# Kernel tuning notes

Measured on AMD Instinct MI355X. Metric: run time of the kernel, lower is better.

The kernel has to match this reference:

```python
import jax, jax.numpy as jnp
import numpy as np

B, IN, HID, EMB, K = 65536, 256, 256, 64, 4096
EPS = 1e-5  # BatchNorm1d default eps


def setup_inputs() -> dict:
    key = jax.random.key(0)
    ks = jax.random.split(key, 12)
    s = 0.05
    return {
        "x": jax.random.normal(ks[0], (B, IN), jnp.float32),
        "W1": jax.random.normal(ks[1], (HID, IN), jnp.float32) * s,
        "b1": jax.random.normal(ks[2], (HID,), jnp.float32) * s,
        "gamma": jnp.ones((HID,), jnp.float32),
        "beta": jnp.zeros((HID,), jnp.float32),
        "mean": jax.random.normal(ks[3], (HID,), jnp.float32) * s,
        "var": jax.random.uniform(ks[4], (HID,), jnp.float32, 0.5, 1.5),
        "W2": jax.random.normal(ks[5], (HID // 2, HID), jnp.float32) * s,
        "b2": jax.random.normal(ks[6], (HID // 2,), jnp.float32) * s,
        "W3": jax.random.normal(ks[7], (EMB, HID // 2), jnp.float32) * s,
        "b3": jax.random.normal(ks[8], (EMB,), jnp.float32) * s,
        "codebook": jax.random.normal(ks[9], (K, EMB), jnp.float32),
    }


def reference(x, W1, b1, gamma, beta, mean, var, W2, b2, W3, b3, codebook):
    # encoder: Linear -> BatchNorm1d (eval stats) -> ReLU -> Linear -> ReLU -> Linear -> Tanh
    h = x @ W1.T + b1                                   # [B, HID]
    h = (h - mean) * jax.lax.rsqrt(var + EPS) * gamma + beta
    h = jax.nn.relu(h)
    h = jax.nn.relu(h @ W2.T + b2)                      # [B, HID//2]
    z = jnp.tanh(h @ W3.T + b3)                         # [B, EMB]
    # squared-distance matrix: ||z||^2 + ||e||^2 - 2 z e^T  -> [B, K]
    d = (jnp.sum(z * z, axis=1, keepdims=True)
         + jnp.sum(codebook * codebook, axis=1)
         - 2.0 * (z @ codebook.T))
    return jnp.argmin(d, axis=1)                        # [B] int token indices
```

## Files before the change

### kernel.cpp

```cpp
#include <hip/hip_runtime.h>

#define IN_DIM  256
#define HID_DIM 256
#define H2_DIM  128
#define EMB_DIM 64
#define K_CODES 4096
#define EPS_BN  1e-5f


typedef _Float16 f16;
typedef _Float16 f16x4 __attribute__((ext_vector_type(4)));
typedef _Float16 f16x8 __attribute__((ext_vector_type(8)));
typedef float    f32x16 __attribute__((ext_vector_type(16)));

__global__ __launch_bounds__(256) void k_norms(const float* __restrict__ cb,
                                               float* __restrict__ norms) {
    int c = blockIdx.x * 256 + threadIdx.x;
    const float4* row = reinterpret_cast<const float4*>(cb + (size_t)c * EMB_DIM);
    float s = 0.f;
#pragma unroll
    for (int i = 0; i < EMB_DIM / 4; ++i) {
        float4 v = row[i];
        s += v.x * v.x + v.y * v.y + v.z * v.z + v.w * v.w;
    }
    norms[c] = 0.5f * s;
}

__global__ __launch_bounds__(256) void k_prep(
    const float* __restrict__ W1, const float* __restrict__ W2,
    const float* __restrict__ W3, const float* __restrict__ cb,
    f16* __restrict__ w1h, f16* __restrict__ w1l,
    f16* __restrict__ w2h, f16* __restrict__ w2l,
    f16* __restrict__ w3h, f16* __restrict__ w3l,
    f16* __restrict__ cbh, f16* __restrict__ cbl) {
    int i = blockIdx.x * 256 + threadIdx.x;
    const float* src; f16 *dh, *dl; int off;
    if (i < 65536)       { src = W1; dh = w1h; dl = w1l; off = i; }
    else if (i < 98304)  { src = W2; dh = w2h; dl = w2l; off = i - 65536; }
    else if (i < 106496) { src = W3; dh = w3h; dl = w3l; off = i - 98304; }
    else                 { src = cb; dh = cbh; dl = cbl; off = i - 106496; }
    float v = src[off];
    f16 h = (f16)v;
    dh[off] = h;
    dl[off] = (f16)(v - (float)h);
}

__global__ __launch_bounds__(256) void k_encoder_mfma(
    const float* __restrict__ x,
    const f16* __restrict__ w1h, const f16* __restrict__ w1l,
    const f16* __restrict__ w2h, const f16* __restrict__ w2l,
    const f16* __restrict__ w3h, const f16* __restrict__ w3l,
    const float* __restrict__ b1,
    const float* __restrict__ gm, const float* __restrict__ bt,
    const float* __restrict__ mu, const float* __restrict__ vr,
    const float* __restrict__ b2, const float* __restrict__ b3,
    f16* __restrict__ Zh, f16* __restrict__ Zl) {
    __shared__ __align__(16) f16 sm[27136];
    const int tid  = threadIdx.x;
    const int lane = tid & 63;
    const int w    = tid >> 6;
    const int ln31 = lane & 31;
    const int q    = lane >> 5;
    const int r0   = blockIdx.x * 32;

    f32x16 acc1a = {};
    f32x16 acc1b = {};
#pragma unroll 1
    for (int kc = 0; kc < 8; ++kc) {
        __syncthreads();
        {
            int row = tid >> 3, c = (tid & 7) * 4;
            float4 v = *reinterpret_cast<const float4*>(
                x + (size_t)(r0 + row) * IN_DIM + kc * 32 + c);
            f16x4 hv, lv;
            hv[0] = (f16)v.x; lv[0] = (f16)(v.x - (float)hv[0]);
            hv[1] = (f16)v.y; lv[1] = (f16)(v.y - (float)hv[1]);
            hv[2] = (f16)v.z; lv[2] = (f16)(v.z - (float)hv[2]);
            hv[3] = (f16)v.w; lv[3] = (f16)(v.w - (float)hv[3]);
            *(f16x4*)(sm + row * 40 + c)        = hv;
            *(f16x4*)(sm + 1280 + row * 40 + c) = lv;
        }
#pragma unroll
        for (int it = 0; it < 4; ++it) {
            int i = it * 256 + tid;
            int j = i >> 2, c8 = (i & 3) * 8;
            *(f16x8*)(sm + 2560 + j * 40 + c8) =
                *(const f16x8*)(w1h + j * IN_DIM + kc * 32 + c8);
            *(f16x8*)(sm + 12800 + j * 40 + c8) =
                *(const f16x8*)(w1l + j * IN_DIM + kc * 32 + c8);
        }
        __syncthreads();
#pragma unroll
        for (int ks = 0; ks < 2; ++ks) {
            f16x8 ah = *(const f16x8*)(sm + ln31 * 40 + ks * 16 + q * 8);
            f16x8 al = *(const f16x8*)(sm + 1280 + ln31 * 40 + ks * 16 + q * 8);
            int j0 = (w * 64 + ln31) * 40 + ks * 16 + q * 8;
            f16x8 bh0 = *(const f16x8*)(sm + 2560 + j0);
            f16x8 bl0 = *(const f16x8*)(sm + 12800 + j0);
            f16x8 bh1 = *(const f16x8*)(sm + 2560 + j0 + 32 * 40);
            f16x8 bl1 = *(const f16x8*)(sm + 12800 + j0 + 32 * 40);
            acc1a = __builtin_amdgcn_mfma_f32_32x32x16_f16(ah, bh0, acc1a, 0, 0, 0);
            acc1b = __builtin_amdgcn_mfma_f32_32x32x16_f16(ah, bh1, acc1b, 0, 0, 0);
            acc1a = __builtin_amdgcn_mfma_f32_32x32x16_f16(al, bh0, acc1a, 0, 0, 0);
            acc1b = __builtin_amdgcn_mfma_f32_32x32x16_f16(al, bh1, acc1b, 0, 0, 0);
            acc1a = __builtin_amdgcn_mfma_f32_32x32x16_f16(ah, bl0, acc1a, 0, 0, 0);
            acc1b = __builtin_amdgcn_mfma_f32_32x32x16_f16(ah, bl1, acc1b, 0, 0, 0);
        }
    }
    __syncthreads();

    {
#pragma unroll
        for (int nt = 0; nt < 2; ++nt) {
            int j = w * 64 + nt * 32 + ln31;
            float sc = gm[j] * rsqrtf(vr[j] + EPS_BN);
            float sh = (b1[j] - mu[j]) * sc + bt[j];
            const f32x16& a = nt ? acc1b : acc1a;
#pragma unroll
            for (int r = 0; r < 16; ++r) {
                int row = (r & 3) + 8 * (r >> 2) + 4 * q;
                float v = a[r] * sc + sh;
                v = v > 0.f ? v : 0.f;
                f16 h = (f16)v;
                sm[row * 264 + j]        = h;
                sm[8448 + row * 264 + j] = (f16)(v - (float)h);
            }
        }
    }

    f32x16 acc2a = {};
    f32x16 acc2b = {};
#pragma unroll 1
    for (int kc = 0; kc < 8; ++kc) {
        __syncthreads();
#pragma unroll
        for (int it = 0; it < 2; ++it) {
            int i = it * 256 + tid;
            int j = i >> 2, c8 = (i & 3) * 8;
            *(f16x8*)(sm + 16896 + j * 40 + c8) =
                *(const f16x8*)(w2h + j * HID_DIM + kc * 32 + c8);
            *(f16x8*)(sm + 22016 + j * 40 + c8) =
                *(const f16x8*)(w2l + j * HID_DIM + kc * 32 + c8);
        }
        __syncthreads();
#pragma unroll
        for (int ks = 0; ks < 2; ++ks) {
            f16x8 ah = *(const f16x8*)(sm + ln31 * 264 + kc * 32 + ks * 16 + q * 8);
            f16x8 al = *(const f16x8*)(sm + 8448 + ln31 * 264 + kc * 32 + ks * 16 + q * 8);
            int j0 = (w * 32 + ln31) * 40 + ks * 16 + q * 8;
            f16x8 bh = *(const f16x8*)(sm + 16896 + j0);
            f16x8 bl = *(const f16x8*)(sm + 22016 + j0);
            f32x16& acc = ks ? acc2b : acc2a;
            acc = __builtin_amdgcn_mfma_f32_32x32x16_f16(ah, bh, acc, 0, 0, 0);
            acc = __builtin_amdgcn_mfma_f32_32x32x16_f16(al, bh, acc, 0, 0, 0);
            acc = __builtin_amdgcn_mfma_f32_32x32x16_f16(ah, bl, acc, 0, 0, 0);
        }
    }
    __syncthreads();

    {
        int j2 = w * 32 + ln31;
        float bias = b2[j2];
#pragma unroll
        for (int r = 0; r < 16; ++r) {
            int row = (r & 3) + 8 * (r >> 2) + 4 * q;
            float v = (acc2a[r] + acc2b[r]) + bias;
            v = v > 0.f ? v : 0.f;
            f16 h = (f16)v;
            sm[row * 136 + j2]        = h;
            sm[4352 + row * 136 + j2] = (f16)(v - (float)h);
        }
#pragma unroll
        for (int it = 0; it < 4; ++it) {
            int i = it * 256 + tid;
            int j = i >> 4, c8 = (i & 15) * 8;
            *(f16x8*)(sm + 8704 + j * 136 + c8) =
                *(const f16x8*)(w3h + j * H2_DIM + c8);
            *(f16x8*)(sm + 17408 + j * 136 + c8) =
                *(const f16x8*)(w3l + j * H2_DIM + c8);
        }
    }
    __syncthreads();

    if (w < 2) {
        f32x16 acc3a = {};
        f32x16 acc3b = {};
#pragma unroll 2
        for (int ks = 0; ks < 8; ++ks) {
            f16x8 ah = *(const f16x8*)(sm + ln31 * 136 + ks * 16 + q * 8);
            f16x8 al = *(const f16x8*)(sm + 4352 + ln31 * 136 + ks * 16 + q * 8);
            int j0 = 8704 + (w * 32 + ln31) * 136 + ks * 16 + q * 8;
            f16x8 bh = *(const f16x8*)(sm + j0);
            f16x8 bl = *(const f16x8*)(sm + j0 + 8704);
            f32x16& acc = (ks & 1) ? acc3b : acc3a;
            acc = __builtin_amdgcn_mfma_f32_32x32x16_f16(ah, bh, acc, 0, 0, 0);
            acc = __builtin_amdgcn_mfma_f32_32x32x16_f16(al, bh, acc, 0, 0, 0);
            acc = __builtin_amdgcn_mfma_f32_32x32x16_f16(ah, bl, acc, 0, 0, 0);
        }
        int j3 = w * 32 + ln31;
        float bias = b3[j3];
#pragma unroll
        for (int r = 0; r < 16; ++r) {
            int row = (r & 3) + 8 * (r >> 2) + 4 * q;
            float zv = tanhf((acc3a[r] + acc3b[r]) + bias);
            f16 h = (f16)zv;
            size_t idx = (size_t)(r0 + row) * EMB_DIM + j3;
            Zh[idx] = h;
            Zl[idx] = (f16)(zv - (float)h);
        }
    }
}

__global__ __launch_bounds__(256) void k_argmin_mfma(
    const f16* __restrict__ Zh, const f16* __restrict__ Zl,
    const f16* __restrict__ cbh, const f16* __restrict__ cbl,
    const float* __restrict__ norms, int* __restrict__ out) {
    __shared__ __align__(16) f16 sm[37120];
    f16* zh  = sm;
    f16* zl  = sm + 9216;
    f16* ebh = sm + 18432;
    f16* ebl = sm + 27648;
    float* nbuf = (float*)(sm + 36864);
    const int tid  = threadIdx.x;
    const int lane = tid & 63;
    const int w    = tid >> 6;
    const int ln31 = lane & 31;
    const int q    = lane >> 5;
    const int r0   = blockIdx.x * 128;

    {
        const float4* srch = (const float4*)(Zh + (size_t)r0 * EMB_DIM);
        const float4* srcl = (const float4*)(Zl + (size_t)r0 * EMB_DIM);
        float4* dsth = (float4*)zh;
        float4* dstl = (float4*)zl;
#pragma unroll
        for (int it = 0; it < 4; ++it) {
            int i = it * 256 + tid;
            int row = i >> 3, c8 = i & 7;
            dsth[row * 9 + c8] = srch[row * 8 + c8];
            dstl[row * 9 + c8] = srcl[row * 8 + c8];
        }
    }
    __syncthreads();

    f16x8 ah[4], al[4];
#pragma unroll
    for (int ks = 0; ks < 4; ++ks) {
        int off = (w * 32 + ln31) * 72 + ks * 16 + q * 8;
        ah[ks] = *(const f16x8*)(zh + off);
        al[ks] = *(const f16x8*)(zl + off);
    }

    float bv[16];
    int   bi[16];
#pragma unroll
    for (int i = 0; i < 16; ++i) { bv[i] = -3.4e38f; bi[i] = 0; }

    for (int ch = 0; ch < K_CODES / 128; ++ch) {
        __syncthreads();
        const float4* srch = (const float4*)(cbh + (size_t)ch * 128 * EMB_DIM);
        const float4* srcl = (const float4*)(cbl + (size_t)ch * 128 * EMB_DIM);
        float4* dsth = (float4*)ebh;
        float4* dstl = (float4*)ebl;
#pragma unroll
        for (int it = 0; it < 4; ++it) {
            int i = it * 256 + tid;
            int row = i >> 3, c8 = i & 7;
            dsth[row * 9 + c8] = srch[row * 8 + c8];
            dstl[row * 9 + c8] = srcl[row * 8 + c8];
        }
        if (tid < 128) nbuf[tid] = norms[ch * 128 + tid];
        __syncthreads();

#pragma unroll 1
        for (int ct = 0; ct < 4; ++ct) {
            f16x8 bh[4], bl[4];
#pragma unroll
            for (int ks = 0; ks < 4; ++ks) {
                int off = (ct * 32 + ln31) * 72 + ks * 16 + q * 8;
                bh[ks] = *(const f16x8*)(ebh + off);
                bl[ks] = *(const f16x8*)(ebl + off);
            }
            f32x16 acc0 = {};
            f32x16 acc1 = {};
#pragma unroll
            for (int ks = 0; ks < 4; ks += 2) {
                acc0 = __builtin_amdgcn_mfma_f32_32x32x16_f16(ah[ks],     bh[ks],     acc0, 0, 0, 0);
                acc1 = __builtin_amdgcn_mfma_f32_32x32x16_f16(ah[ks + 1], bh[ks + 1], acc1, 0, 0, 0);
                acc0 = __builtin_amdgcn_mfma_f32_32x32x16_f16(al[ks],     bh[ks],     acc0, 0, 0, 0);
                acc1 = __builtin_amdgcn_mfma_f32_32x32x16_f16(al[ks + 1], bh[ks + 1], acc1, 0, 0, 0);
                acc0 = __builtin_amdgcn_mfma_f32_32x32x16_f16(ah[ks],     bl[ks],     acc0, 0, 0, 0);
                acc1 = __builtin_amdgcn_mfma_f32_32x32x16_f16(ah[ks + 1], bl[ks + 1], acc1, 0, 0, 0);
            }
            float nv  = nbuf[ct * 32 + ln31];
            int   col = ch * 128 + ct * 32 + ln31;
#pragma unroll
            for (int r = 0; r < 16; ++r) {
                float t  = (acc0[r] + acc1[r]) - nv;
                bool  gt = t > bv[r];
                bv[r] = gt ? t : bv[r];
                bi[r] = gt ? col : bi[r];
            }
        }
    }

    __syncthreads();
    float* redv = (float*)(sm + 18432);
    int*   redi = (int*)(sm + 18432) + 4224;
#pragma unroll
    for (int r = 0; r < 16; ++r) {
        int row = (r & 3) + 8 * (r >> 2) + 4 * q + 32 * w;
        redv[row * 33 + ln31] = bv[r];
        redi[row * 33 + ln31] = bi[r];
    }
    __syncthreads();
    if (tid < 128) {
        float v  = redv[tid * 33];
        int   ix = redi[tid * 33];
#pragma unroll
        for (int j = 1; j < 32; ++j) {
            float vj = redv[tid * 33 + j];
            int   ij = redi[tid * 33 + j];
            if (vj > v) { v = vj; ix = ij; }
        }
        out[r0 + tid] = ix;
    }
}

extern "C" void kernel_launch(void* const* d_in, const int* in_sizes, int n_in,
                              void* d_out, int out_size, void* d_ws, size_t ws_size,
                              hipStream_t stream) {
    (void)n_in; (void)out_size; (void)ws_size;
    const float* x  = (const float*)d_in[0];
    const float* W1 = (const float*)d_in[1];
    const float* b1 = (const float*)d_in[2];
    const float* gm = (const float*)d_in[3];
    const float* bt = (const float*)d_in[4];
    const float* mu = (const float*)d_in[5];
    const float* vr = (const float*)d_in[6];
    const float* W2 = (const float*)d_in[7];
    const float* b2 = (const float*)d_in[8];
    const float* W3 = (const float*)d_in[9];
    const float* b3 = (const float*)d_in[10];
    const float* cb = (const float*)d_in[11];

    char* ws = (char*)d_ws;
    float* norms = (float*)ws;
    f16* cbh = (f16*)(ws + 16384);
    f16* cbl = (f16*)(ws + 540672);
    f16* w1h = (f16*)(ws + 1064960);
    f16* w1l = (f16*)(ws + 1196032);
    f16* w2h = (f16*)(ws + 1327104);
    f16* w2l = (f16*)(ws + 1392640);
    f16* w3h = (f16*)(ws + 1458176);
    f16* w3l = (f16*)(ws + 1474560);
    f16* Zh  = (f16*)(ws + 1490944);
    f16* Zl  = (f16*)(ws + 9879552);
    int* out = (int*)d_out;

    const int B = in_sizes[0] / IN_DIM;

    k_norms<<<K_CODES / 256, 256, 0, stream>>>(cb, norms);
    k_prep<<<1440, 256, 0, stream>>>(W1, W2, W3, cb, w1h, w1l, w2h, w2l,
                                     w3h, w3l, cbh, cbl);
    k_encoder_mfma<<<B / 32, 256, 0, stream>>>(x, w1h, w1l, w2h, w2l, w3h, w3l,
                                               b1, gm, bt, mu, vr, b2, b3, Zh, Zl);
    k_argmin_mfma<<<B / 128, 256, 0, stream>>>(Zh, Zl, cbh, cbl, norms, out);
}
```

Baseline: 295.2 us.

## Pre-pack weights and codebook into MFMA fragment layout, load B operands directly

```diff
diff --git a/kernel.cpp b/kernel.cpp
--- a/kernel.cpp
+++ b/kernel.cpp
@@ -29,33 +29,57 @@
 __global__ __launch_bounds__(256) void k_prep(
     const float* __restrict__ W1, const float* __restrict__ W2,
     const float* __restrict__ W3, const float* __restrict__ cb,
-    f16* __restrict__ w1h, f16* __restrict__ w1l,
-    f16* __restrict__ w2h, f16* __restrict__ w2l,
-    f16* __restrict__ w3h, f16* __restrict__ w3l,
-    f16* __restrict__ cbh, f16* __restrict__ cbl) {
-    int i = blockIdx.x * 256 + threadIdx.x;
-    const float* src; f16 *dh, *dl; int off;
-    if (i < 65536)       { src = W1; dh = w1h; dl = w1l; off = i; }
-    else if (i < 98304)  { src = W2; dh = w2h; dl = w2l; off = i - 65536; }
-    else if (i < 106496) { src = W3; dh = w3h; dl = w3l; off = i - 98304; }
-    else                 { src = cb; dh = cbh; dl = cbl; off = i - 106496; }
-    float v = src[off];
-    f16 h = (f16)v;
-    dh[off] = h;
-    dl[off] = (f16)(v - (float)h);
+    f16* __restrict__ p1h, f16* __restrict__ p1l,
+    f16* __restrict__ p2h, f16* __restrict__ p2l,
+    f16* __restrict__ p3h, f16* __restrict__ p3l,
+    f16* __restrict__ cfh, f16* __restrict__ cfl) {
+    int t = blockIdx.x * 256 + threadIdx.x;
+    const float* src; f16 *dh, *dl; int tt, row, k0, K;
+    if (t < 8192) {
+        tt = t; int f = tt >> 6, l = tt & 63;
+        int ct = f & 7, kst = f >> 3;
+        row = ct * 32 + (l & 31); k0 = kst * 16 + (l >> 5) * 8;
+        src = W1; K = IN_DIM; dh = p1h; dl = p1l;
+    } else if (t < 12288) {
+        tt = t - 8192; int f = tt >> 6, l = tt & 63;
+        int ct = f & 3, kst = f >> 2;
+        row = ct * 32 + (l & 31); k0 = kst * 16 + (l >> 5) * 8;
+        src = W2; K = HID_DIM; dh = p2h; dl = p2l;
+    } else if (t < 13312) {
+        tt = t - 12288; int f = tt >> 6, l = tt & 63;
+        int ct = f & 1, ks = f >> 1;
+        row = ct * 32 + (l & 31); k0 = ks * 16 + (l >> 5) * 8;
+        src = W3; K = H2_DIM; dh = p3h; dl = p3l;
+    } else {
+        tt = t - 13312; int f = tt >> 6, l = tt & 63;
+        int ct = f & 3, ks = (f >> 2) & 3, ch = f >> 4;
+        row = ch * 128 + ct * 32 + (l & 31); k0 = ks * 16 + (l >> 5) * 8;
+        src = cb; K = EMB_DIM; dh = cfh; dl = cfl;
+    }
+    const float* s = src + (size_t)row * K + k0;
+    f16x8 hv, lv;
+#pragma unroll
+    for (int j = 0; j < 8; ++j) {
+        float v = s[j];
+        f16 h = (f16)v;
+        hv[j] = h;
+        lv[j] = (f16)(v - (float)h);
+    }
+    *(f16x8*)(dh + (size_t)tt * 8) = hv;
+    *(f16x8*)(dl + (size_t)tt * 8) = lv;
 }
 
 __global__ __launch_bounds__(256) void k_encoder_mfma(
     const float* __restrict__ x,
-    const f16* __restrict__ w1h, const f16* __restrict__ w1l,
-    const f16* __restrict__ w2h, const f16* __restrict__ w2l,
-    const f16* __restrict__ w3h, const f16* __restrict__ w3l,
+    const f16* __restrict__ p1h, const f16* __restrict__ p1l,
+    const f16* __restrict__ p2h, const f16* __restrict__ p2l,
+    const f16* __restrict__ p3h, const f16* __restrict__ p3l,
     const float* __restrict__ b1,
     const float* __restrict__ gm, const float* __restrict__ bt,
     const float* __restrict__ mu, const float* __restrict__ vr,
     const float* __restrict__ b2, const float* __restrict__ b3,
     f16* __restrict__ Zh, f16* __restrict__ Zl) {
-    __shared__ __align__(16) f16 sm[27136];
+    __shared__ __align__(16) f16 sm[25600];
     const int tid  = threadIdx.x;
     const int lane = tid & 63;
     const int w    = tid >> 6;
@@ -63,49 +87,41 @@
     const int q    = lane >> 5;
     const int r0   = blockIdx.x * 32;
 
+#pragma unroll
+    for (int it = 0; it < 8; ++it) {
+        int i = it * 256 + tid;
+        int row = i >> 6, c4 = (i & 63) * 4;
+        float4 v = *reinterpret_cast<const float4*>(
+            x + (size_t)(r0 + row) * IN_DIM + c4);
+        f16x4 hv, lv;
+        hv[0] = (f16)v.x; lv[0] = (f16)(v.x - (float)hv[0]);
+        hv[1] = (f16)v.y; lv[1] = (f16)(v.y - (float)hv[1]);
+        hv[2] = (f16)v.z; lv[2] = (f16)(v.z - (float)hv[2]);
+        hv[3] = (f16)v.w; lv[3] = (f16)(v.w - (float)hv[3]);
+        *(f16x4*)(sm + row * 264 + c4)        = hv;
+        *(f16x4*)(sm + 8448 + row * 264 + c4) = lv;
+    }
+    __syncthreads();
+
     f32x16 acc1a = {};
     f32x16 acc1b = {};
-#pragma unroll 1
-    for (int kc = 0; kc < 8; ++kc) {
-        __syncthreads();
-        {
-            int row = tid >> 3, c = (tid & 7) * 4;
-            float4 v = *reinterpret_cast<const float4*>(
-                x + (size_t)(r0 + row) * IN_DIM + kc * 32 + c);
-            f16x4 hv, lv;
-            hv[0] = (f16)v.x; lv[0] = (f16)(v.x - (float)hv[0]);
-            hv[1] = (f16)v.y; lv[1] = (f16)(v.y - (float)hv[1]);
-            hv[2] = (f16)v.z; lv[2] = (f16)(v.z - (float)hv[2]);
-            hv[3] = (f16)v.w; lv[3] = (f16)(v.w - (float)hv[3]);
-            *(f16x4*)(sm + row * 40 + c)        = hv;
-            *(f16x4*)(sm + 1280 + row * 40 + c) = lv;
-        }
-#pragma unroll
-        for (int it = 0; it < 4; ++it) {
-            int i = it * 256 + tid;
-            int j = i >> 2, c8 = (i & 3) * 8;
-            *(f16x8*)(sm + 2560 + j * 40 + c8) =
-                *(const f16x8*)(w1h + j * IN_DIM + kc * 32 + c8);
-            *(f16x8*)(sm + 12800 + j * 40 + c8) =
-                *(const f16x8*)(w1l + j * IN_DIM + kc * 32 + c8);
-        }
-        __syncthreads();
-#pragma unroll
-        for (int ks = 0; ks < 2; ++ks) {
-            f16x8 ah = *(const f16x8*)(sm + ln31 * 40 + ks * 16 + q * 8);
-            f16x8 al = *(const f16x8*)(sm + 1280 + ln31 * 40 + ks * 16 + q * 8);
-            int j0 = (w * 64 + ln31) * 40 + ks * 16 + q * 8;
-            f16x8 bh0 = *(const f16x8*)(sm + 2560 + j0);
-            f16x8 bl0 = *(const f16x8*)(sm + 12800 + j0);
-            f16x8 bh1 = *(const f16x8*)(sm + 2560 + j0 + 32 * 40);
-            f16x8 bl1 = *(const f16x8*)(sm + 12800 + j0 + 32 * 40);
-            acc1a = __builtin_amdgcn_mfma_f32_32x32x16_f16(ah, bh0, acc1a, 0, 0, 0);
-            acc1b = __builtin_amdgcn_mfma_f32_32x32x16_f16(ah, bh1, acc1b, 0, 0, 0);
-            acc1a = __builtin_amdgcn_mfma_f32_32x32x16_f16(al, bh0, acc1a, 0, 0, 0);
-            acc1b = __builtin_amdgcn_mfma_f32_32x32x16_f16(al, bh1, acc1b, 0, 0, 0);
-            acc1a = __builtin_amdgcn_mfma_f32_32x32x16_f16(ah, bl0, acc1a, 0, 0, 0);
-            acc1b = __builtin_amdgcn_mfma_f32_32x32x16_f16(ah, bl1, acc1b, 0, 0, 0);
-        }
+#pragma unroll 2
+    for (int kst = 0; kst < 16; ++kst) {
+        int koff = kst * 16 + q * 8;
+        f16x8 ah = *(const f16x8*)(sm + ln31 * 264 + koff);
+        f16x8 al = *(const f16x8*)(sm + 8448 + ln31 * 264 + koff);
+        const f16* pbh = p1h + (size_t)(kst * 8 + 2 * w) * 512 + lane * 8;
+        const f16* pbl = p1l + (size_t)(kst * 8 + 2 * w) * 512 + lane * 8;
+        f16x8 bh0 = *(const f16x8*)pbh;
+        f16x8 bh1 = *(const f16x8*)(pbh + 512);
+        f16x8 bl0 = *(const f16x8*)pbl;
+        f16x8 bl1 = *(const f16x8*)(pbl + 512);
+        acc1a = __builtin_amdgcn_mfma_f32_32x32x16_f16(ah, bh0, acc1a, 0, 0, 0);
+        acc1b = __builtin_amdgcn_mfma_f32_32x32x16_f16(ah, bh1, acc1b, 0, 0, 0);
+        acc1a = __builtin_amdgcn_mfma_f32_32x32x16_f16(al, bh0, acc1a, 0, 0, 0);
+        acc1b = __builtin_amdgcn_mfma_f32_32x32x16_f16(al, bh1, acc1b, 0, 0, 0);
+        acc1a = __builtin_amdgcn_mfma_f32_32x32x16_f16(ah, bl0, acc1a, 0, 0, 0);
+        acc1b = __builtin_amdgcn_mfma_f32_32x32x16_f16(ah, bl1, acc1b, 0, 0, 0);
     }
     __syncthreads();
 
@@ -127,37 +143,24 @@
             }
         }
     }
+    __syncthreads();
 
     f32x16 acc2a = {};
     f32x16 acc2b = {};
-#pragma unroll 1
-    for (int kc = 0; kc < 8; ++kc) {
-        __syncthreads();
-#pragma unroll
-        for (int it = 0; it < 2; ++it) {
-            int i = it * 256 + tid;
-            int j = i >> 2, c8 = (i & 3) * 8;
-            *(f16x8*)(sm + 16896 + j * 40 + c8) =
-                *(const f16x8*)(w2h + j * HID_DIM + kc * 32 + c8);
-            *(f16x8*)(sm + 22016 + j * 40 + c8) =
-                *(const f16x8*)(w2l + j * HID_DIM + kc * 32 + c8);
-        }
-        __syncthreads();
-#pragma unroll
-        for (int ks = 0; ks < 2; ++ks) {
-            f16x8 ah = *(const f16x8*)(sm + ln31 * 264 + kc * 32 + ks * 16 + q * 8);
-            f16x8 al = *(const f16x8*)(sm + 8448 + ln31 * 264 + kc * 32 + ks * 16 + q * 8);
-            int j0 = (w * 32 + ln31) * 40 + ks * 16 + q * 8;
-            f16x8 bh = *(const f16x8*)(sm + 16896 + j0);
-            f16x8 bl = *(const f16x8*)(sm + 22016 + j0);
-            f32x16& acc = ks ? acc2b : acc2a;
-            acc = __builtin_amdgcn_mfma_f32_32x32x16_f16(ah, bh, acc, 0, 0, 0);
-            acc = __builtin_amdgcn_mfma_f32_32x32x16_f16(al, bh, acc, 0, 0, 0);
-            acc = __builtin_amdgcn_mfma_f32_32x32x16_f16(ah, bl, acc, 0, 0, 0);
-        }
-    }
-    __syncthreads();
-
+#pragma unroll 2
+    for (int kst = 0; kst < 16; ++kst) {
+        int koff = kst * 16 + q * 8;
+        f16x8 ah = *(const f16x8*)(sm + ln31 * 264 + koff);
+        f16x8 al = *(const f16x8*)(sm + 8448 + ln31 * 264 + koff);
+        const f16* pbh = p2h + (size_t)(kst * 4 + w) * 512 + lane * 8;
+        const f16* pbl = p2l + (size_t)(kst * 4 + w) * 512 + lane * 8;
+        f16x8 bh = *(const f16x8*)pbh;
+        f16x8 bl = *(const f16x8*)pbl;
+        f32x16& acc = (kst & 1) ? acc2b : acc2a;
+        acc = __builtin_amdgcn_mfma_f32_32x32x16_f16(ah, bh, acc, 0, 0, 0);
+        acc = __builtin_amdgcn_mfma_f32_32x32x16_f16(al, bh, acc, 0, 0, 0);
+        acc = __builtin_amdgcn_mfma_f32_32x32x16_f16(ah, bl, acc, 0, 0, 0);
+    }
     {
         int j2 = w * 32 + ln31;
         float bias = b2[j2];
@@ -167,17 +170,8 @@
             float v = (acc2a[r] + acc2b[r]) + bias;
             v = v > 0.f ? v : 0.f;
             f16 h = (f16)v;
-            sm[row * 136 + j2]        = h;
-            sm[4352 + row * 136 + j2] = (f16)(v - (float)h);
-        }
-#pragma unroll
-        for (int it = 0; it < 4; ++it) {
-            int i = it * 256 + tid;
-            int j = i >> 4, c8 = (i & 15) * 8;
-            *(f16x8*)(sm + 8704 + j * 136 + c8) =
-                *(const f16x8*)(w3h + j * H2_DIM + c8);
-            *(f16x8*)(sm + 17408 + j * 136 + c8) =
-                *(const f16x8*)(w3l + j * H2_DIM + c8);
+            sm[16896 + row * 136 + j2] = h;
+            sm[21248 + row * 136 + j2] = (f16)(v - (float)h);
         }
     }
     __syncthreads();
@@ -187,11 +181,12 @@
         f32x16 acc3b = {};
 #pragma unroll 2
         for (int ks = 0; ks < 8; ++ks) {
-            f16x8 ah = *(const f16x8*)(sm + ln31 * 136 + ks * 16 + q * 8);
-            f16x8 al = *(const f16x8*)(sm + 4352 + ln31 * 136 + ks * 16 + q * 8);
-            int j0 = 8704 + (w * 32 + ln31) * 136 + ks * 16 + q * 8;
-            f16x8 bh = *(const f16x8*)(sm + j0);
-            f16x8 bl = *(const f16x8*)(sm + j0 + 8704);
+            f16x8 ah = *(const f16x8*)(sm + 16896 + ln31 * 136 + ks * 16 + q * 8);
+            f16x8 al = *(const f16x8*)(sm + 21248 + ln31 * 136 + ks * 16 + q * 8);
+            const f16* pbh = p3h + (size_t)(ks * 2 + w) * 512 + lane * 8;
+            const f16* pbl = p3l + (size_t)(ks * 2 + w) * 512 + lane * 8;
+            f16x8 bh = *(const f16x8*)pbh;
+            f16x8 bl = *(const f16x8*)pbl;
             f32x16& acc = (ks & 1) ? acc3b : acc3a;
             acc = __builtin_amdgcn_mfma_f32_32x32x16_f16(ah, bh, acc, 0, 0, 0);
             acc = __builtin_amdgcn_mfma_f32_32x32x16_f16(al, bh, acc, 0, 0, 0);
@@ -213,14 +208,12 @@
 
 __global__ __launch_bounds__(256) void k_argmin_mfma(
     const f16* __restrict__ Zh, const f16* __restrict__ Zl,
-    const f16* __restrict__ cbh, const f16* __restrict__ cbl,
+    const f16* __restrict__ cfh, const f16* __restrict__ cfl,
     const float* __restrict__ norms, int* __restrict__ out) {
-    __shared__ __align__(16) f16 sm[37120];
-    f16* zh  = sm;
-    f16* zl  = sm + 9216;
-    f16* ebh = sm + 18432;
-    f16* ebl = sm + 27648;
-    float* nbuf = (float*)(sm + 36864);
+    __shared__ __align__(16) f16 sm[16896];
+    f16* ebh = sm;
+    f16* ebl = sm + 8192;
+    float* nbuf = (float*)(sm + 16384);
     const int tid  = threadIdx.x;
     const int lane = tid & 63;
     const int w    = tid >> 6;
@@ -228,27 +221,12 @@
     const int q    = lane >> 5;
     const int r0   = blockIdx.x * 128;
 
-    {
-        const float4* srch = (const float4*)(Zh + (size_t)r0 * EMB_DIM);
-        const float4* srcl = (const float4*)(Zl + (size_t)r0 * EMB_DIM);
-        float4* dsth = (float4*)zh;
-        float4* dstl = (float4*)zl;
-#pragma unroll
-        for (int it = 0; it < 4; ++it) {
-            int i = it * 256 + tid;
-            int row = i >> 3, c8 = i & 7;
-            dsth[row * 9 + c8] = srch[row * 8 + c8];
-            dstl[row * 9 + c8] = srcl[row * 8 + c8];
-        }
-    }
-    __syncthreads();
-
     f16x8 ah[4], al[4];
 #pragma unroll
     for (int ks = 0; ks < 4; ++ks) {
-        int off = (w * 32 + ln31) * 72 + ks * 16 + q * 8;
-        ah[ks] = *(const f16x8*)(zh + off);
-        al[ks] = *(const f16x8*)(zl + off);
+        size_t zoff = (size_t)(r0 + w * 32 + ln31) * EMB_DIM + ks * 16 + q * 8;
+        ah[ks] = *(const f16x8*)(Zh + zoff);
+        al[ks] = *(const f16x8*)(Zl + zoff);
     }
 
     float bv[16];
@@ -258,16 +236,14 @@
 
     for (int ch = 0; ch < K_CODES / 128; ++ch) {
         __syncthreads();
-        const float4* srch = (const float4*)(cbh + (size_t)ch * 128 * EMB_DIM);
-        const float4* srcl = (const float4*)(cbl + (size_t)ch * 128 * EMB_DIM);
-        float4* dsth = (float4*)ebh;
-        float4* dstl = (float4*)ebl;
+        const float4* sh = (const float4*)(cfh + (size_t)ch * 8192);
+        const float4* sl = (const float4*)(cfl + (size_t)ch * 8192);
+        float4* dh = (float4*)ebh;
+        float4* dl = (float4*)ebl;
 #pragma unroll
         for (int it = 0; it < 4; ++it) {
-            int i = it * 256 + tid;
-            int row = i >> 3, c8 = i & 7;
-            dsth[row * 9 + c8] = srch[row * 8 + c8];
-            dstl[row * 9 + c8] = srcl[row * 8 + c8];
+            dh[it * 256 + tid] = sh[it * 256 + tid];
+            dl[it * 256 + tid] = sl[it * 256 + tid];
         }
         if (tid < 128) nbuf[tid] = norms[ch * 128 + tid];
         __syncthreads();
@@ -277,7 +253,7 @@
             f16x8 bh[4], bl[4];
 #pragma unroll
             for (int ks = 0; ks < 4; ++ks) {
-                int off = (ct * 32 + ln31) * 72 + ks * 16 + q * 8;
+                int off = (ks * 4 + ct) * 512 + lane * 8;
                 bh[ks] = *(const f16x8*)(ebh + off);
                 bl[ks] = *(const f16x8*)(ebl + off);
             }
@@ -305,8 +281,8 @@
     }
 
     __syncthreads();
-    float* redv = (float*)(sm + 18432);
-    int*   redi = (int*)(sm + 18432) + 4224;
+    float* redv = (float*)sm;
+    int*   redi = (int*)sm + 4224;
 #pragma unroll
     for (int r = 0; r < 16; ++r) {
         int row = (r & 3) + 8 * (r >> 2) + 4 * q + 32 * w;
@@ -346,14 +322,14 @@
 
     char* ws = (char*)d_ws;
     float* norms = (float*)ws;
-    f16* cbh = (f16*)(ws + 16384);
-    f16* cbl = (f16*)(ws + 540672);
-    f16* w1h = (f16*)(ws + 1064960);
-    f16* w1l = (f16*)(ws + 1196032);
-    f16* w2h = (f16*)(ws + 1327104);
-    f16* w2l = (f16*)(ws + 1392640);
-    f16* w3h = (f16*)(ws + 1458176);
-    f16* w3l = (f16*)(ws + 1474560);
+    f16* cfh = (f16*)(ws + 16384);
+    f16* cfl = (f16*)(ws + 540672);
+    f16* p1h = (f16*)(ws + 1064960);
+    f16* p1l = (f16*)(ws + 1196032);
+    f16* p2h = (f16*)(ws + 1327104);
+    f16* p2l = (f16*)(ws + 1392640);
+    f16* p3h = (f16*)(ws + 1458176);
+    f16* p3l = (f16*)(ws + 1474560);
     f16* Zh  = (f16*)(ws + 1490944);
     f16* Zl  = (f16*)(ws + 9879552);
     int* out = (int*)d_out;
@@ -361,9 +337,9 @@
     const int B = in_sizes[0] / IN_DIM;
 
     k_norms<<<K_CODES / 256, 256, 0, stream>>>(cb, norms);
-    k_prep<<<1440, 256, 0, stream>>>(W1, W2, W3, cb, w1h, w1l, w2h, w2l,
-                                     w3h, w3l, cbh, cbl);
-    k_encoder_mfma<<<B / 32, 256, 0, stream>>>(x, w1h, w1l, w2h, w2l, w3h, w3l,
+    k_prep<<<180, 256, 0, stream>>>(W1, W2, W3, cb, p1h, p1l, p2h, p2l,
+                                    p3h, p3l, cfh, cfl);
+    k_encoder_mfma<<<B / 32, 256, 0, stream>>>(x, p1h, p1l, p2h, p2l, p3h, p3l,
                                                b1, gm, bt, mu, vr, b2, b3, Zh, Zl);
-    k_argmin_mfma<<<B / 128, 256, 0, stream>>>(Zh, Zl, cbh, cbl, norms, out);
-}
+    k_argmin_mfma<<<B / 128, 256, 0, stream>>>(Zh, Zl, cfh, cfl, norms, out);
+}
```

Result: no change. 294.6 us (-0.2%).
